# Optimization experiments

Measured on AMD Instinct MI355X. Metric: run time of the kernel, lower is better.

Reference implementation:

```python
import jax, jax.numpy as jnp
import numpy as np

EMBED_DIM = 1024
NUM_HEADS = 16
D_K = EMBED_DIM // NUM_HEADS
MAX_SEQ = 2048
BATCH = 2
SEQ = 2048
ROPE_BASE = 10000.0


def build_rope(seq_len, head_dim, base=ROPE_BASE):
    # standard RoPE: inv_freq over half the head dim, cos/sin of shape [seq, head_dim]
    inv_freq = 1.0 / (base ** (jnp.arange(0, head_dim, 2, dtype=jnp.float32) / head_dim))
    t = jnp.arange(seq_len, dtype=jnp.float32)
    freqs = jnp.einsum('s,d->sd', t, inv_freq)              # [S, D/2]
    emb = jnp.concatenate([freqs, freqs], axis=-1)          # [S, D]
    return jnp.cos(emb), jnp.sin(emb)


def rotate_half(x):
    x1, x2 = jnp.split(x, 2, axis=-1)
    return jnp.concatenate([-x2, x1], axis=-1)


def apply_rope(x, cos, sin):
    # x: [B, H, S, D]; cos/sin: [S, D] -> broadcast over batch & heads
    cos = cos[None, None, :, :]
    sin = sin[None, None, :, :]
    return x * cos + rotate_half(x) * sin


def setup_inputs() -> dict:
    key = jax.random.key(0)
    ks = jax.random.split(key, 9)
    scale = 1.0 / np.sqrt(EMBED_DIM)
    x = jax.random.normal(ks[0], (BATCH, SEQ, EMBED_DIM), dtype=jnp.float32)
    # causal boolean mask, broadcastable to [B, H, S, S]
    mask = jnp.tril(jnp.ones((SEQ, SEQ), dtype=bool))[None, None, :, :]
    cos, sin = build_rope(MAX_SEQ, D_K)
    Wq = jax.random.normal(ks[1], (EMBED_DIM, EMBED_DIM), jnp.float32) * scale
    bq = jnp.zeros((EMBED_DIM,), jnp.float32)
    Wk = jax.random.normal(ks[2], (EMBED_DIM, EMBED_DIM), jnp.float32) * scale
    bk = jnp.zeros((EMBED_DIM,), jnp.float32)
    Wv = jax.random.normal(ks[3], (EMBED_DIM, EMBED_DIM), jnp.float32) * scale
    bv = jnp.zeros((EMBED_DIM,), jnp.float32)
    Wo = jax.random.normal(ks[4], (EMBED_DIM, EMBED_DIM), jnp.float32) * scale
    bo = jnp.zeros((EMBED_DIM,), jnp.float32)
    return {'x': x, 'mask': mask, 'cos': cos, 'sin': sin,
            'Wq': Wq, 'bq': bq, 'Wk': Wk, 'bk': bk, 'Wv': Wv, 'bv': bv,
            'Wo': Wo, 'bo': bo}


def reference(x, mask, cos, sin, Wq, bq, Wk, bk, Wv, bv, Wo, bo):
    B, S, E = x.shape
    H, D = NUM_HEADS, D_K
    # nn.Linear: y = x @ W^T + b
    q = (x @ Wq.T + bq).reshape(B, S, H, D).transpose(0, 2, 1, 3)  # [B,H,S,D]
    k = (x @ Wk.T + bk).reshape(B, S, H, D).transpose(0, 2, 1, 3)
    v = (x @ Wv.T + bv).reshape(B, S, H, D).transpose(0, 2, 1, 3)
    q = apply_rope(q, cos[:S], sin[:S])
    k = apply_rope(k, cos[:S], sin[:S])
    scores = jnp.einsum('bhqd,bhkd->bhqk', q, k) / jnp.sqrt(jnp.float32(D))
    scores = jnp.where(mask, scores, -jnp.inf)
    attn = jax.nn.softmax(scores, axis=-1)
    out = jnp.einsum('bhqk,bhkd->bhqd', attn, v)
    out = out.transpose(0, 2, 1, 3).reshape(B, S, E)
    return out @ Wo.T + bo
```

## Files before the change

### kernel.cpp

```cpp
#include <hip/hip_runtime.h>
#include <hip/hip_bf16.h>
#include <cfloat>
#include <math.h>

#define EMBED 1024
#define NHEADS 16
#define DK 64
#define SEQL 2048
#define BATCH 2
#define NTOK 4096


typedef __bf16 bf16x8 __attribute__((ext_vector_type(8)));
typedef float floatx4 __attribute__((ext_vector_type(4)));

__device__ __forceinline__ unsigned short f2bf(float f) {
    union { __hip_bfloat16 b; unsigned short u; } c;
    c.b = __float2bfloat16(f);
    return c.u;
}

__device__ __forceinline__ void async16(void* lds, const void* g) {
    __builtin_amdgcn_global_load_lds(
        (const __attribute__((address_space(1))) unsigned int*)g,
        (__attribute__((address_space(3))) unsigned int*)lds,
        16, 0, 0);
}

__global__ __launch_bounds__(256) void convert_pack(
    const float* __restrict__ x,  const float* __restrict__ Wq,
    const float* __restrict__ Wk, const float* __restrict__ Wv,
    const float* __restrict__ Wo,
    unsigned short* __restrict__ xb, unsigned short* __restrict__ Wqkv,
    unsigned short* __restrict__ Wob)
{
    const int XG = 1048576, WG = 262144;
    int g = blockIdx.x * 256 + threadIdx.x;
    const float4* s; ushort4* d;
    if (g < XG)               { s = (const float4*)x  + g;                d = (ushort4*)xb   + g; }
    else if (g < XG + WG)     { s = (const float4*)Wq + (g - XG);         d = (ushort4*)Wqkv + (g - XG); }
    else if (g < XG + 2 * WG) { s = (const float4*)Wk + (g - XG - WG);    d = (ushort4*)Wqkv + (g - XG); }
    else if (g < XG + 3 * WG) { s = (const float4*)Wv + (g - XG - 2*WG);  d = (ushort4*)Wqkv + (g - XG); }
    else                      { s = (const float4*)Wo + (g - XG - 3*WG);  d = (ushort4*)Wob  + (g - XG - 3*WG); }
    float4 v = *s;
    *d = (ushort4){f2bf(v.x), f2bf(v.y), f2bf(v.z), f2bf(v.w)};
}

__global__ __launch_bounds__(256) void qkv_gemm(
    const unsigned short* __restrict__ xb, const unsigned short* __restrict__ Wqkv,
    const float* __restrict__ bq, const float* __restrict__ bk, const float* __restrict__ bv,
    const float* __restrict__ cosT, const float* __restrict__ sinT,
    unsigned short* __restrict__ Qg, unsigned short* __restrict__ Kg,
    unsigned short* __restrict__ Vt)
{
    __shared__ __align__(16) unsigned short SM[9216];
    unsigned short* As = SM;
    unsigned short* Bs = SM + 4096;

    const int t = threadIdx.x, lane = t & 63, wave = t >> 6;
    const int quad = lane >> 4, lrow = lane & 15;
    const int m0 = blockIdx.y * 128;
    const int n0 = blockIdx.x * 128;
    const int mw = (wave & 1) * 64, nw = (wave >> 1) * 64;
    const int srow = lane >> 2;
    const int scol = (lane & 3) * 8;

    floatx4 acc[4][4];
    #pragma unroll
    for (int i = 0; i < 4; i++)
        #pragma unroll
        for (int j = 0; j < 4; j++) acc[i][j] = (floatx4){0.f,0.f,0.f,0.f};

    const unsigned short* Ab = xb   + (size_t)(m0 + wave * 32 + srow) * EMBED + scol;
    const unsigned short* Bb = Wqkv + (size_t)(n0 + wave * 32 + srow) * EMBED + scol;

    for (int k0 = 0; k0 < EMBED; k0 += 32) {
        __syncthreads();
        async16(&As[wave * 1024],       Ab + k0);
        async16(&As[wave * 1024 + 512], Ab + 16 * EMBED + k0);
        async16(&Bs[wave * 1024],       Bb + k0);
        async16(&Bs[wave * 1024 + 512], Bb + 16 * EMBED + k0);
        __syncthreads();

        bf16x8 af[4], bfB[4];
        #pragma unroll
        for (int i = 0; i < 4; i++)
            af[i] = *reinterpret_cast<const bf16x8*>(&As[(mw + i * 16 + lrow) * 32 + quad * 8]);
        #pragma unroll
        for (int j = 0; j < 4; j++)
            bfB[j] = *reinterpret_cast<const bf16x8*>(&Bs[(nw + j * 16 + lrow) * 32 + quad * 8]);
        #pragma unroll
        for (int i = 0; i < 4; i++)
            #pragma unroll
            for (int j = 0; j < 4; j++)
                acc[i][j] = __builtin_amdgcn_mfma_f32_16x16x32_bf16(af[i], bfB[j], acc[i][j], 0, 0, 0);
    }

    const int mat  = n0 >> 10;
    const int nloc = n0 & 1023;
    const int bb   = m0 >> 11;
    const int s0   = m0 & (SEQL - 1);

    for (int hn = 0; hn < 2; hn++) {
        const int h = (nloc >> 6) + hn;
        __syncthreads();
        if (mat == 2) {
            unsigned short* T2 = SM;
            if ((wave >> 1) == hn) {
                #pragma unroll
                for (int j = 0; j < 4; j++) {
                    int d = j * 16 + lrow;
                    float bvv = bv[nloc + hn * 64 + d];
                    #pragma unroll
                    for (int i = 0; i < 4; i++) {
                        int tok = mw + i * 16 + quad * 4;
                        *(ushort4*)&T2[d * 136 + tok] = (ushort4){
                            f2bf(acc[i][j][0] + bvv), f2bf(acc[i][j][1] + bvv),
                            f2bf(acc[i][j][2] + bvv), f2bf(acc[i][j][3] + bvv)};
                    }
                }
            }
            __syncthreads();
            int d = t >> 2, tg = (t & 3) * 32;
            unsigned short* dst = Vt + ((size_t)(bb * NHEADS + h) * DK + d) * SEQL + s0 + tg;
            #pragma unroll
            for (int c = 0; c < 32; c += 8)
                *(uint4*)(dst + c) = *(const uint4*)&T2[d * 136 + tg + c];
        } else {
            unsigned short* T = SM;
            const float* bias = (mat == 0) ? bq : bk;
            if ((wave >> 1) == hn) {
                #pragma unroll
                for (int j = 0; j < 4; j++) {
                    int d = j * 16 + lrow;
                    float bvv = bias[nloc + hn * 64 + d];
                    #pragma unroll
                    for (int i = 0; i < 4; i++)
                        #pragma unroll
                        for (int rg = 0; rg < 4; rg++)
                            T[(mw + i * 16 + quad * 4 + rg) * 72 + d] = f2bf(acc[i][j][rg] + bvv);
                }
            }
            __syncthreads();
            int tok = t >> 1, dh = (t & 1) * 32;
            int s = s0 + tok;
            float sgn = dh ? 1.0f : -1.0f;
            unsigned short* dst = ((mat == 0) ? Qg : Kg)
                + ((size_t)(bb * NHEADS + h) * SEQL + s) * DK + dh;
            #pragma unroll
            for (int c = 0; c < 32; c += 8) {
                bf16x8 own = *reinterpret_cast<const bf16x8*>(&T[tok * 72 + dh + c]);
                bf16x8 par = *reinterpret_cast<const bf16x8*>(&T[tok * 72 + (dh ^ 32) + c]);
                float4 c0 = *(const float4*)(cosT + s * DK + dh + c);
                float4 c1 = *(const float4*)(cosT + s * DK + dh + c + 4);
                float4 s0v = *(const float4*)(sinT + s * DK + dh + c);
                float4 s1v = *(const float4*)(sinT + s * DK + dh + c + 4);
                float cv[8] = {c0.x,c0.y,c0.z,c0.w,c1.x,c1.y,c1.z,c1.w};
                float sv[8] = {s0v.x,s0v.y,s0v.z,s0v.w,s1v.x,s1v.y,s1v.z,s1v.w};
                unsigned short o[8];
                #pragma unroll
                for (int e = 0; e < 8; e++)
                    o[e] = f2bf((float)own[e] * cv[e] + sgn * (float)par[e] * sv[e]);
                *(uint4*)(dst + c) = *(const uint4*)o;
            }
        }
    }
}

#define KP 72

__global__ __launch_bounds__(256) void attn_mfma(
    const unsigned short* __restrict__ Qg, const unsigned short* __restrict__ Kg,
    const unsigned short* __restrict__ Vt, unsigned short* __restrict__ CTX)
{
    __shared__ __align__(16) unsigned short Ks[64 * KP];
    __shared__ __align__(16) unsigned short Vs[64 * KP];
    __shared__ __align__(16) unsigned short Ps[64 * KP];

    const int p = blockIdx.x;
    const int h = blockIdx.y, b = blockIdx.z;
    const int qtL = p, qtH = (SEQL / 64 - 1) - p;
    const int t = threadIdx.x;
    const int lane = t & 63, w = t >> 6;
    const int quad = lane >> 4, lrow = lane & 15;
    const int q0L = qtL * 64, q0H = qtH * 64;

    const unsigned short* Qh = Qg + (size_t)(b * NHEADS + h) * SEQL * DK;
    const unsigned short* Kh = Kg + (size_t)(b * NHEADS + h) * SEQL * DK;
    const unsigned short* Vh = Vt + (size_t)(b * NHEADS + h) * DK * SEQL;

    bf16x8 aqL[2], aqH[2];
    #pragma unroll
    for (int ks = 0; ks < 2; ks++) {
        aqL[ks] = *(const bf16x8*)(Qh + (size_t)(q0L + w * 16 + lrow) * DK + quad * 8 + ks * 32);
        aqH[ks] = *(const bf16x8*)(Qh + (size_t)(q0H + w * 16 + lrow) * DK + quad * 8 + ks * 32);
    }

    floatx4 ofL[4], ofH[4];
    float lL[4] = {0,0,0,0}, lH[4] = {0,0,0,0};
    #pragma unroll
    for (int jd = 0; jd < 4; jd++) { ofL[jd] = (floatx4){0,0,0,0}; ofH[jd] = (floatx4){0,0,0,0}; }

    unsigned short* Pw = Ps + w * 16 * KP;

    const int r0 = t >> 3, c8 = (t & 7) * 8;
    uint4 pk0, pk1, pv0, pv1;
    auto pref = [&](int k0) {
        pk0 = *(const uint4*)(Kh + (size_t)(k0 + r0) * DK + c8);
        pk1 = *(const uint4*)(Kh + (size_t)(k0 + r0 + 32) * DK + c8);
        pv0 = *(const uint4*)(Vh + (size_t)r0 * SEQL + k0 + c8);
        pv1 = *(const uint4*)(Vh + (size_t)(r0 + 32) * SEQL + k0 + c8);
    };
    pref(0);

    for (int kt = 0; kt <= qtH; kt++) {
        const int k0 = kt * 64;
        __syncthreads();
        *(uint4*)&Ks[r0 * KP + c8]        = pk0;
        *(uint4*)&Ks[(r0 + 32) * KP + c8] = pk1;
        *(uint4*)&Vs[r0 * KP + c8]        = pv0;
        *(uint4*)&Vs[(r0 + 32) * KP + c8] = pv1;
        __syncthreads();
        if (kt < qtH) pref(k0 + 64);

        {
            floatx4 sc[4];
            #pragma unroll
            for (int j = 0; j < 4; j++) sc[j] = (floatx4){0,0,0,0};
            #pragma unroll
            for (int ks = 0; ks < 2; ks++)
                #pragma unroll
                for (int j = 0; j < 4; j++) {
                    bf16x8 kb = *reinterpret_cast<const bf16x8*>(&Ks[(j * 16 + lrow) * KP + quad * 8 + ks * 32]);
                    sc[j] = __builtin_amdgcn_mfma_f32_16x16x32_bf16(aqH[ks], kb, sc[j], 0, 0, 0);
                }
            const bool diag = (kt == qtH);
            #pragma unroll
            for (int rg = 0; rg < 4; rg++) {
                int row = q0H + w * 16 + quad * 4 + rg;
                float lacc = 0.f;
                #pragma unroll
                for (int j = 0; j < 4; j++) {
                    float pval = __expf(sc[j][rg] * 0.125f);
                    if (diag && (k0 + j * 16 + lrow) > row) pval = 0.f;
                    Pw[(quad * 4 + rg) * KP + j * 16 + lrow] = f2bf(pval);
                    lacc += pval;
                }
                lH[rg] += lacc;
            }
            #pragma unroll
            for (int ks = 0; ks < 2; ks++) {
                bf16x8 pa = *reinterpret_cast<const bf16x8*>(&Pw[lrow * KP + quad * 8 + ks * 32]);
                #pragma unroll
                for (int jd = 0; jd < 4; jd++) {
                    bf16x8 vb = *reinterpret_cast<const bf16x8*>(&Vs[(jd * 16 + lrow) * KP + quad * 8 + ks * 32]);
                    ofH[jd] = __builtin_amdgcn_mfma_f32_16x16x32_bf16(pa, vb, ofH[jd], 0, 0, 0);
                }
            }
        }
        if (kt <= qtL) {
            floatx4 sc[4];
            #pragma unroll
            for (int j = 0; j < 4; j++) sc[j] = (floatx4){0,0,0,0};
            #pragma unroll
            for (int ks = 0; ks < 2; ks++)
                #pragma unroll
                for (int j = 0; j < 4; j++) {
                    bf16x8 kb = *reinterpret_cast<const bf16x8*>(&Ks[(j * 16 + lrow) * KP + quad * 8 + ks * 32]);
                    sc[j] = __builtin_amdgcn_mfma_f32_16x16x32_bf16(aqL[ks], kb, sc[j], 0, 0, 0);
                }
            const bool diag = (kt == qtL);
            #pragma unroll
            for (int rg = 0; rg < 4; rg++) {
                int row = q0L + w * 16 + quad * 4 + rg;
                float lacc = 0.f;
                #pragma unroll
                for (int j = 0; j < 4; j++) {
                    float pval = __expf(sc[j][rg] * 0.125f);
                    if (diag && (k0 + j * 16 + lrow) > row) pval = 0.f;
                    Pw[(quad * 4 + rg) * KP + j * 16 + lrow] = f2bf(pval);
                    lacc += pval;
                }
                lL[rg] += lacc;
            }
            #pragma unroll
            for (int ks = 0; ks < 2; ks++) {
                bf16x8 pa = *reinterpret_cast<const bf16x8*>(&Pw[lrow * KP + quad * 8 + ks * 32]);
                #pragma unroll
                for (int jd = 0; jd < 4; jd++) {
                    bf16x8 vb = *reinterpret_cast<const bf16x8*>(&Vs[(jd * 16 + lrow) * KP + quad * 8 + ks * 32]);
                    ofL[jd] = __builtin_amdgcn_mfma_f32_16x16x32_bf16(pa, vb, ofL[jd], 0, 0, 0);
                }
            }
        }
    }

    #pragma unroll
    for (int rg = 0; rg < 4; rg++) {
        float lv = lH[rg];
        #pragma unroll
        for (int off = 1; off < 16; off <<= 1) lv += __shfl_xor(lv, off);
        float inv = 1.0f / lv;
        int row = q0H + w * 16 + quad * 4 + rg;
        unsigned short* Cr = CTX + ((size_t)(b * NHEADS + h) * SEQL + row) * DK;
        #pragma unroll
        for (int jd = 0; jd < 4; jd++) Cr[jd * 16 + lrow] = f2bf(ofH[jd][rg] * inv);

        lv = lL[rg];
        #pragma unroll
        for (int off = 1; off < 16; off <<= 1) lv += __shfl_xor(lv, off);
        inv = 1.0f / lv;
        row = q0L + w * 16 + quad * 4 + rg;
        Cr = CTX + ((size_t)(b * NHEADS + h) * SEQL + row) * DK;
        #pragma unroll
        for (int jd = 0; jd < 4; jd++) Cr[jd * 16 + lrow] = f2bf(ofL[jd][rg] * inv);
    }
}

__global__ __launch_bounds__(256) void o_gemm(
    const unsigned short* __restrict__ Ag,
    const unsigned short* __restrict__ Bg,
    const float* __restrict__ bias, float* __restrict__ C)
{
    __shared__ __align__(16) unsigned short As[128 * 32];
    __shared__ __align__(16) unsigned short Bs[128 * 32];

    const int t = threadIdx.x, lane = t & 63, wave = t >> 6;
    const int quad = lane >> 4, lrow = lane & 15;
    const int m0 = blockIdx.y * 128, n0 = blockIdx.x * 128;
    const int mw = (wave & 1) * 64, nw = (wave >> 1) * 64;
    const int srow = lane >> 2;
    const int scol = (lane & 3) * 8;

    floatx4 acc[4][4];
    #pragma unroll
    for (int i = 0; i < 4; i++)
        #pragma unroll
        for (int j = 0; j < 4; j++) acc[i][j] = (floatx4){0.f,0.f,0.f,0.f};

    const int tokA0 = m0 + wave * 32 + srow;
    const unsigned short* Bb = Bg + (size_t)(n0 + wave * 32 + srow) * EMBED + scol;

    for (int k0 = 0; k0 < EMBED; k0 += 32) {
        int k = k0 + scol;
        size_t a0 = ((size_t)((tokA0 >> 11) * NHEADS + (k >> 6)) * SEQL + (tokA0 & (SEQL - 1))) * DK + (k & 63);
        int tokA1 = tokA0 + 16;
        size_t a1 = ((size_t)((tokA1 >> 11) * NHEADS + (k >> 6)) * SEQL + (tokA1 & (SEQL - 1))) * DK + (k & 63);
        __syncthreads();
        async16(&As[wave * 1024],       Ag + a0);
        async16(&As[wave * 1024 + 512], Ag + a1);
        async16(&Bs[wave * 1024],       Bb + k0);
        async16(&Bs[wave * 1024 + 512], Bb + 16 * EMBED + k0);
        __syncthreads();

        bf16x8 af[4], bfB[4];
        #pragma unroll
        for (int i = 0; i < 4; i++)
            af[i] = *reinterpret_cast<const bf16x8*>(&As[(mw + i * 16 + lrow) * 32 + quad * 8]);
        #pragma unroll
        for (int j = 0; j < 4; j++)
            bfB[j] = *reinterpret_cast<const bf16x8*>(&Bs[(nw + j * 16 + lrow) * 32 + quad * 8]);
        #pragma unroll
        for (int i = 0; i < 4; i++)
            #pragma unroll
            for (int j = 0; j < 4; j++)
                acc[i][j] = __builtin_amdgcn_mfma_f32_16x16x32_bf16(af[i], bfB[j], acc[i][j], 0, 0, 0);
    }

    #pragma unroll
    for (int i = 0; i < 4; i++)
        #pragma unroll
        for (int rg = 0; rg < 4; rg++) {
            int row_g = m0 + mw + i * 16 + quad * 4 + rg;
            #pragma unroll
            for (int j = 0; j < 4; j++) {
                int col_g = n0 + nw + j * 16 + lrow;
                C[(size_t)row_g * EMBED + col_g] = acc[i][j][rg] + bias[col_g];
            }
        }
}

extern "C" void kernel_launch(void* const* d_in, const int* in_sizes, int n_in,
                              void* d_out, int out_size, void* d_ws, size_t ws_size,
                              hipStream_t stream) {
    const float* x    = (const float*)d_in[0];
    const float* cosT = (const float*)d_in[2];
    const float* sinT = (const float*)d_in[3];
    const float* Wq = (const float*)d_in[4];  const float* bq = (const float*)d_in[5];
    const float* Wk = (const float*)d_in[6];  const float* bk = (const float*)d_in[7];
    const float* Wv = (const float*)d_in[8];  const float* bv = (const float*)d_in[9];
    const float* Wo = (const float*)d_in[10]; const float* bo = (const float*)d_in[11];

    const size_t MB = 1024 * 1024;
    char* ws = (char*)d_ws;
    unsigned short* xb   = (unsigned short*)(ws);
    unsigned short* Wqkv = (unsigned short*)(ws +  8 * MB);
    unsigned short* Wob  = (unsigned short*)(ws + 14 * MB);
    unsigned short* Qg   = (unsigned short*)(ws + 16 * MB);
    unsigned short* Kg   = (unsigned short*)(ws + 24 * MB);
    unsigned short* Vt   = (unsigned short*)(ws + 32 * MB);
    unsigned short* CTXb = (unsigned short*)(ws + 40 * MB);

    convert_pack<<<8192, 256, 0, stream>>>(x, Wq, Wk, Wv, Wo, xb, Wqkv, Wob);

    dim3 qkv_grid(3 * EMBED / 128, NTOK / 128);
    qkv_gemm<<<qkv_grid, 256, 0, stream>>>(xb, Wqkv, bq, bk, bv, cosT, sinT, Qg, Kg, Vt);

    dim3 attn_grid(SEQL / 128, NHEADS, BATCH);
    attn_mfma<<<attn_grid, 256, 0, stream>>>(Qg, Kg, Vt, CTXb);

    dim3 o_grid(EMBED / 128, NTOK / 128);
    o_gemm<<<o_grid, 256, 0, stream>>>(CTXb, Wob, bo, (float*)d_out);
}
```

Measured before the change: 255.7 us.

## Double K-step in GEMMs and widen attention KV tile to 128 keys

The QKV and output-projection GEMMs now stage 64 elements of K per barrier pair (two 32-wide LDS sub-tiles) instead of 32, halving the number of synchronisation rounds. The attention kernel now processes 128 keys per iteration, with eight score fragments per wave and wider padded V and P tiles, halving the loop trip count and barriers. In exchange, LDS use per block grows, which may reduce occupancy. Register pressure also rises from more prefetch registers and score accumulators. The diagonal tile can also do up to 64 keys of fully masked, wasted work.

```diff
diff --git a/kernel.cpp b/kernel.cpp
--- a/kernel.cpp
+++ b/kernel.cpp
@@ -53,9 +53,11 @@
     unsigned short* __restrict__ Qg, unsigned short* __restrict__ Kg,
     unsigned short* __restrict__ Vt)
 {
-    __shared__ __align__(16) unsigned short SM[9216];
-    unsigned short* As = SM;
-    unsigned short* Bs = SM + 4096;
+    __shared__ __align__(16) unsigned short SM[16384];
+    unsigned short* As0 = SM;
+    unsigned short* As1 = SM + 4096;
+    unsigned short* Bs0 = SM + 8192;
+    unsigned short* Bs1 = SM + 12288;
 
     const int t = threadIdx.x, lane = t & 63, wave = t >> 6;
     const int quad = lane >> 4, lrow = lane & 15;
@@ -71,29 +73,36 @@
         #pragma unroll
         for (int j = 0; j < 4; j++) acc[i][j] = (floatx4){0.f,0.f,0.f,0.f};
 
-    const unsigned short* Ab = xb   + (size_t)(m0 + wave * 32 + srow) * EMBED + scol;
-    const unsigned short* Bb = Wqkv + (size_t)(n0 + wave * 32 + srow) * EMBED + scol;
-
-    for (int k0 = 0; k0 < EMBED; k0 += 32) {
-        __syncthreads();
-        async16(&As[wave * 1024],       Ab + k0);
-        async16(&As[wave * 1024 + 512], Ab + 16 * EMBED + k0);
-        async16(&Bs[wave * 1024],       Bb + k0);
-        async16(&Bs[wave * 1024 + 512], Bb + 16 * EMBED + k0);
-        __syncthreads();
-
-        bf16x8 af[4], bfB[4];
-        #pragma unroll
-        for (int i = 0; i < 4; i++)
-            af[i] = *reinterpret_cast<const bf16x8*>(&As[(mw + i * 16 + lrow) * 32 + quad * 8]);
-        #pragma unroll
-        for (int j = 0; j < 4; j++)
-            bfB[j] = *reinterpret_cast<const bf16x8*>(&Bs[(nw + j * 16 + lrow) * 32 + quad * 8]);
-        #pragma unroll
-        for (int i = 0; i < 4; i++)
+    for (int k0 = 0; k0 < EMBED; k0 += 64) {
+        __syncthreads();
+        #pragma unroll
+        for (int c = 0; c < 2; c++) {
+            const unsigned short* as = xb   + (size_t)(m0 + wave * 32 + c * 16 + srow) * EMBED + k0 + scol;
+            const unsigned short* bs = Wqkv + (size_t)(n0 + wave * 32 + c * 16 + srow) * EMBED + k0 + scol;
+            async16(&As0[wave * 1024 + c * 512], as);
+            async16(&As1[wave * 1024 + c * 512], as + 32);
+            async16(&Bs0[wave * 1024 + c * 512], bs);
+            async16(&Bs1[wave * 1024 + c * 512], bs + 32);
+        }
+        __syncthreads();
+
+        #pragma unroll
+        for (int ks = 0; ks < 2; ks++) {
+            const unsigned short* Ab = ks ? As1 : As0;
+            const unsigned short* Bb = ks ? Bs1 : Bs0;
+            bf16x8 af[4], bfB[4];
+            #pragma unroll
+            for (int i = 0; i < 4; i++)
+                af[i] = *reinterpret_cast<const bf16x8*>(&Ab[(mw + i * 16 + lrow) * 32 + quad * 8]);
             #pragma unroll
             for (int j = 0; j < 4; j++)
-                acc[i][j] = __builtin_amdgcn_mfma_f32_16x16x32_bf16(af[i], bfB[j], acc[i][j], 0, 0, 0);
+                bfB[j] = *reinterpret_cast<const bf16x8*>(&Bb[(nw + j * 16 + lrow) * 32 + quad * 8]);
+            #pragma unroll
+            for (int i = 0; i < 4; i++)
+                #pragma unroll
+                for (int j = 0; j < 4; j++)
+                    acc[i][j] = __builtin_amdgcn_mfma_f32_16x16x32_bf16(af[i], bfB[j], acc[i][j], 0, 0, 0);
+        }
     }
 
     const int mat  = n0 >> 10;
@@ -168,14 +177,15 @@
 }
 
 #define KP 72
+#define VP 136
 
 __global__ __launch_bounds__(256) void attn_mfma(
     const unsigned short* __restrict__ Qg, const unsigned short* __restrict__ Kg,
     const unsigned short* __restrict__ Vt, unsigned short* __restrict__ CTX)
 {
-    __shared__ __align__(16) unsigned short Ks[64 * KP];
-    __shared__ __align__(16) unsigned short Vs[64 * KP];
-    __shared__ __align__(16) unsigned short Ps[64 * KP];
+    __shared__ __align__(16) unsigned short Ks[128 * KP];
+    __shared__ __align__(16) unsigned short Vs[64 * VP];
+    __shared__ __align__(16) unsigned short Ps[64 * VP];
 
     const int p = blockIdx.x;
     const int h = blockIdx.y, b = blockIdx.z;
@@ -184,6 +194,7 @@
     const int lane = t & 63, w = t >> 6;
     const int quad = lane >> 4, lrow = lane & 15;
     const int q0L = qtL * 64, q0H = qtH * 64;
+    const int ktHmax = qtH >> 1, ktLmax = qtL >> 1;
 
     const unsigned short* Qh = Qg + (size_t)(b * NHEADS + h) * SEQL * DK;
     const unsigned short* Kh = Kg + (size_t)(b * NHEADS + h) * SEQL * DK;
@@ -201,94 +212,97 @@
     #pragma unroll
     for (int jd = 0; jd < 4; jd++) { ofL[jd] = (floatx4){0,0,0,0}; ofH[jd] = (floatx4){0,0,0,0}; }
 
-    unsigned short* Pw = Ps + w * 16 * KP;
-
-    const int r0 = t >> 3, c8 = (t & 7) * 8;
-    uint4 pk0, pk1, pv0, pv1;
+    unsigned short* Pw = Ps + w * 16 * VP;
+
+    const int kr = t >> 3, kc8 = (t & 7) * 8;
+    const int vr = t >> 4, vc8 = (t & 15) * 8;
+    uint4 pk[4], pv[4];
     auto pref = [&](int k0) {
-        pk0 = *(const uint4*)(Kh + (size_t)(k0 + r0) * DK + c8);
-        pk1 = *(const uint4*)(Kh + (size_t)(k0 + r0 + 32) * DK + c8);
-        pv0 = *(const uint4*)(Vh + (size_t)r0 * SEQL + k0 + c8);
-        pv1 = *(const uint4*)(Vh + (size_t)(r0 + 32) * SEQL + k0 + c8);
+        #pragma unroll
+        for (int n = 0; n < 4; n++) {
+            pk[n] = *(const uint4*)(Kh + (size_t)(k0 + kr + 32 * n) * DK + kc8);
+            pv[n] = *(const uint4*)(Vh + (size_t)(vr + 16 * n) * SEQL + k0 + vc8);
+        }
     };
     pref(0);
 
-    for (int kt = 0; kt <= qtH; kt++) {
-        const int k0 = kt * 64;
-        __syncthreads();
-        *(uint4*)&Ks[r0 * KP + c8]        = pk0;
-        *(uint4*)&Ks[(r0 + 32) * KP + c8] = pk1;
-        *(uint4*)&Vs[r0 * KP + c8]        = pv0;
-        *(uint4*)&Vs[(r0 + 32) * KP + c8] = pv1;
-        __syncthreads();
-        if (kt < qtH) pref(k0 + 64);
+    for (int kt = 0; kt <= ktHmax; kt++) {
+        const int k0 = kt * 128;
+        __syncthreads();
+        #pragma unroll
+        for (int n = 0; n < 4; n++) {
+            *(uint4*)&Ks[(kr + 32 * n) * KP + kc8] = pk[n];
+            *(uint4*)&Vs[(vr + 16 * n) * VP + vc8] = pv[n];
+        }
+        __syncthreads();
+        if (kt < ktHmax) pref(k0 + 128);
 
         {
-            floatx4 sc[4];
-            #pragma unroll
-            for (int j = 0; j < 4; j++) sc[j] = (floatx4){0,0,0,0};
+            floatx4 sc[8];
+            #pragma unroll
+            for (int j = 0; j < 8; j++) sc[j] = (floatx4){0,0,0,0};
             #pragma unroll
             for (int ks = 0; ks < 2; ks++)
                 #pragma unroll
-                for (int j = 0; j < 4; j++) {
+                for (int j = 0; j < 8; j++) {
                     bf16x8 kb = *reinterpret_cast<const bf16x8*>(&Ks[(j * 16 + lrow) * KP + quad * 8 + ks * 32]);
                     sc[j] = __builtin_amdgcn_mfma_f32_16x16x32_bf16(aqH[ks], kb, sc[j], 0, 0, 0);
                 }
-            const bool diag = (kt == qtH);
+            const bool diag = (kt == ktHmax);
             #pragma unroll
             for (int rg = 0; rg < 4; rg++) {
                 int row = q0H + w * 16 + quad * 4 + rg;
                 float lacc = 0.f;
                 #pragma unroll
-                for (int j = 0; j < 4; j++) {
+                for (int j = 0; j < 8; j++) {
                     float pval = __expf(sc[j][rg] * 0.125f);
                     if (diag && (k0 + j * 16 + lrow) > row) pval = 0.f;
-                    Pw[(quad * 4 + rg) * KP + j * 16 + lrow] = f2bf(pval);
+                    Pw[(quad * 4 + rg) * VP + j * 16 + lrow] = f2bf(pval);
                     lacc += pval;
                 }
                 lH[rg] += lacc;
             }
             #pragma unroll
-            for (int ks = 0; ks < 2; ks++) {
-                bf16x8 pa = *reinterpret_cast<const bf16x8*>(&Pw[lrow * KP + quad * 8 + ks * 32]);
+            for (int ks = 0; ks < 4; ks++) {
+                bf16x8 pa = *reinterpret_cast<const bf16x8*>(&Pw[lrow * VP + quad * 8 + ks * 32]);
                 #pragma unroll
                 for (int jd = 0; jd < 4; jd++) {
-                    bf16x8 vb = *reinterpret_cast<const bf16x8*>(&Vs[(jd * 16 + lrow) * KP + quad * 8 + ks * 32]);
+                    bf16x8 vb = *reinterpret_cast<const bf16x8*>(&Vs[(jd * 16 + lrow) * VP + quad * 8 + ks * 32]);
                     ofH[jd] = __builtin_amdgcn_mfma_f32_16x16x32_bf16(pa, vb, ofH[jd], 0, 0, 0);
                 }
             }
         }
-        if (kt <= qtL) {
-            floatx4 sc[4];
-            #pragma unroll
-            for (int j = 0; j < 4; j++) sc[j] = (floatx4){0,0,0,0};
+        if (kt <= ktLmax) {
+            floatx4 sc[8];
+            #pragma unroll
+            for (int j = 0; j < 8; j++) sc[j] = (floatx4){0,0,0,0};
             #pragma unroll
             for (int ks = 0; ks < 2; ks++)
                 #pragma unroll
-                for (int j = 0; j < 4; j++) {
+                for (int j = 0; j < 8; j++) {
                     bf16x8 kb = *reinterpret_cast<const bf16x8*>(&Ks[(j * 16 + lrow) * KP + quad * 8 + ks * 32]);
                     sc[j] = __builtin_amdgcn_mfma_f32_16x16x32_bf16(aqL[ks], kb, sc[j], 0, 0, 0);
                 }
-            const bool diag = (kt == qtL);
+            const bool diag = (kt == ktLmax);
             #pragma unroll
             for (int rg = 0; rg < 4; rg++) {
                 int row = q0L + w * 16 + quad * 4 + rg;
                 float lacc = 0.f;
                 #pragma unroll
-                for (int j = 0; j < 4; j++) {
+                for (int j = 0; j < 8; j++) {
                     float pval = __expf(sc[j][rg] * 0.125f);
                     if (diag && (k0 + j * 16 + lrow) > row) pval = 0.f;
-                    Pw[(quad * 4 + rg) * KP + j * 16 + lrow] = f2bf(pval);
+                    Pw[(quad * 4 + rg) * VP + j * 16 + lrow] = f2bf(pval);
                     lacc += pval;
                 }
                 lL[rg] += lacc;
             }
             #pragma unroll
-            for (int ks = 0; ks < 2; ks++) {
-                bf16x8 pa = *reinterpret_cast<const bf16x8*>(&Pw[lrow * KP + quad * 8 + ks * 32]);
+            for (int ks = 0; ks < 4; ks++) {
+                bf16x8 pa = *reinterpret_cast<const bf16x8*>(&Pw[lrow * VP + quad * 8 + ks * 32]);
                 #pragma unroll
                 for (int jd = 0; jd < 4; jd++) {
-                    bf16x8 vb = *reinterpret_cast<const bf16x8*>(&Vs[(jd * 16 + lrow) * KP + quad * 8 + ks * 32]);
+                    bf16x8 vb = *reinterpret_cast<const bf16x8*>(&Vs[(jd * 16 + lrow) * VP + quad * 8 + ks * 32]);
                     ofL[jd] = __builtin_amdgcn_mfma_f32_16x16x32_bf16(pa, vb, ofL[jd], 0, 0, 0);
                 }
             }
@@ -322,8 +336,11 @@
     const unsigned short* __restrict__ Bg,
     const float* __restrict__ bias, float* __restrict__ C)
 {
-    __shared__ __align__(16) unsigned short As[128 * 32];
-    __shared__ __align__(16) unsigned short Bs[128 * 32];
+    __shared__ __align__(16) unsigned short SM[16384];
+    unsigned short* As0 = SM;
+    unsigned short* As1 = SM + 4096;
+    unsigned short* Bs0 = SM + 8192;
+    unsigned short* Bs1 = SM + 12288;
 
     const int t = threadIdx.x, lane = t & 63, wave = t >> 6;
     const int quad = lane >> 4, lrow = lane & 15;
@@ -338,33 +355,39 @@
         #pragma unroll
         for (int j = 0; j < 4; j++) acc[i][j] = (floatx4){0.f,0.f,0.f,0.f};
 
-    const int tokA0 = m0 + wave * 32 + srow;
-    const unsigned short* Bb = Bg + (size_t)(n0 + wave * 32 + srow) * EMBED + scol;
-
-    for (int k0 = 0; k0 < EMBED; k0 += 32) {
-        int k = k0 + scol;
-        size_t a0 = ((size_t)((tokA0 >> 11) * NHEADS + (k >> 6)) * SEQL + (tokA0 & (SEQL - 1))) * DK + (k & 63);
-        int tokA1 = tokA0 + 16;
-        size_t a1 = ((size_t)((tokA1 >> 11) * NHEADS + (k >> 6)) * SEQL + (tokA1 & (SEQL - 1))) * DK + (k & 63);
-        __syncthreads();
-        async16(&As[wave * 1024],       Ag + a0);
-        async16(&As[wave * 1024 + 512], Ag + a1);
-        async16(&Bs[wave * 1024],       Bb + k0);
-        async16(&Bs[wave * 1024 + 512], Bb + 16 * EMBED + k0);
-        __syncthreads();
-
-        bf16x8 af[4], bfB[4];
-        #pragma unroll
-        for (int i = 0; i < 4; i++)
-            af[i] = *reinterpret_cast<const bf16x8*>(&As[(mw + i * 16 + lrow) * 32 + quad * 8]);
-        #pragma unroll
-        for (int j = 0; j < 4; j++)
-            bfB[j] = *reinterpret_cast<const bf16x8*>(&Bs[(nw + j * 16 + lrow) * 32 + quad * 8]);
-        #pragma unroll
-        for (int i = 0; i < 4; i++)
+    for (int k0 = 0; k0 < EMBED; k0 += 64) {
+        const int hh = k0 >> 6;
+        __syncthreads();
+        #pragma unroll
+        for (int c = 0; c < 2; c++) {
+            int tok = m0 + wave * 32 + c * 16 + srow;
+            const unsigned short* as = Ag
+                + ((size_t)((tok >> 11) * NHEADS + hh) * SEQL + (tok & (SEQL - 1))) * DK + scol;
+            const unsigned short* bs = Bg + (size_t)(n0 + wave * 32 + c * 16 + srow) * EMBED + k0 + scol;
+            async16(&As0[wave * 1024 + c * 512], as);
+            async16(&As1[wave * 1024 + c * 512], as + 32);
+            async16(&Bs0[wave * 1024 + c * 512], bs);
+            async16(&Bs1[wave * 1024 + c * 512], bs + 32);
+        }
+        __syncthreads();
+
+        #pragma unroll
+        for (int ks = 0; ks < 2; ks++) {
+            const unsigned short* Ab = ks ? As1 : As0;
+            const unsigned short* Bb = ks ? Bs1 : Bs0;
+            bf16x8 af[4], bfB[4];
+            #pragma unroll
+            for (int i = 0; i < 4; i++)
+                af[i] = *reinterpret_cast<const bf16x8*>(&Ab[(mw + i * 16 + lrow) * 32 + quad * 8]);
             #pragma unroll
             for (int j = 0; j < 4; j++)
-                acc[i][j] = __builtin_amdgcn_mfma_f32_16x16x32_bf16(af[i], bfB[j], acc[i][j], 0, 0, 0);
+                bfB[j] = *reinterpret_cast<const bf16x8*>(&Bb[(nw + j * 16 + lrow) * 32 + quad * 8]);
+            #pragma unroll
+            for (int i = 0; i < 4; i++)
+                #pragma unroll
+                for (int j = 0; j < 4; j++)
+                    acc[i][j] = __builtin_amdgcn_mfma_f32_16x16x32_bf16(af[i], bfB[j], acc[i][j], 0, 0, 0);
+        }
     }
 
     #pragma unroll
```

After: 290.4 us. 13.6% more time.

## Shrink GEMM tiles to 128x64 with K=64 steps and unpair attention query tiles

Applied to the files above, without the earlier changes.

Both GEMMs move from 128x128 tiles with K-step 32 to 128x64 tiles with K-step 64. This doubles the block count and halves the number of barrier pairs per K. The attention kernel no longer pairs a low and a high query tile per block; each block handles one 64-row tile, longest first. The grid doubles, raising occupancy and parallelism on the large CU count, at the cost of less data reuse per block and a load imbalance that the reversed launch order is meant to offset.

```diff
diff --git a/kernel.cpp b/kernel.cpp
--- a/kernel.cpp
+++ b/kernel.cpp
@@ -53,116 +53,118 @@
     unsigned short* __restrict__ Qg, unsigned short* __restrict__ Kg,
     unsigned short* __restrict__ Vt)
 {
-    __shared__ __align__(16) unsigned short SM[9216];
-    unsigned short* As = SM;
-    unsigned short* Bs = SM + 4096;
+    __shared__ __align__(16) unsigned short SM[12288];
+    unsigned short* As0 = SM;
+    unsigned short* As1 = SM + 4096;
+    unsigned short* Bs0 = SM + 8192;
+    unsigned short* Bs1 = SM + 10240;
 
     const int t = threadIdx.x, lane = t & 63, wave = t >> 6;
     const int quad = lane >> 4, lrow = lane & 15;
     const int m0 = blockIdx.y * 128;
-    const int n0 = blockIdx.x * 128;
-    const int mw = (wave & 1) * 64, nw = (wave >> 1) * 64;
+    const int n0 = blockIdx.x * 64;
     const int srow = lane >> 2;
     const int scol = (lane & 3) * 8;
 
-    floatx4 acc[4][4];
-    #pragma unroll
-    for (int i = 0; i < 4; i++)
+    floatx4 acc[2][4];
+    #pragma unroll
+    for (int i = 0; i < 2; i++)
         #pragma unroll
         for (int j = 0; j < 4; j++) acc[i][j] = (floatx4){0.f,0.f,0.f,0.f};
 
-    const unsigned short* Ab = xb   + (size_t)(m0 + wave * 32 + srow) * EMBED + scol;
-    const unsigned short* Bb = Wqkv + (size_t)(n0 + wave * 32 + srow) * EMBED + scol;
-
-    for (int k0 = 0; k0 < EMBED; k0 += 32) {
-        __syncthreads();
-        async16(&As[wave * 1024],       Ab + k0);
-        async16(&As[wave * 1024 + 512], Ab + 16 * EMBED + k0);
-        async16(&Bs[wave * 1024],       Bb + k0);
-        async16(&Bs[wave * 1024 + 512], Bb + 16 * EMBED + k0);
-        __syncthreads();
-
-        bf16x8 af[4], bfB[4];
-        #pragma unroll
-        for (int i = 0; i < 4; i++)
-            af[i] = *reinterpret_cast<const bf16x8*>(&As[(mw + i * 16 + lrow) * 32 + quad * 8]);
-        #pragma unroll
-        for (int j = 0; j < 4; j++)
-            bfB[j] = *reinterpret_cast<const bf16x8*>(&Bs[(nw + j * 16 + lrow) * 32 + quad * 8]);
-        #pragma unroll
-        for (int i = 0; i < 4; i++)
+    for (int k0 = 0; k0 < EMBED; k0 += 64) {
+        __syncthreads();
+        #pragma unroll
+        for (int c = 0; c < 2; c++) {
+            const unsigned short* as = xb + (size_t)(m0 + wave * 32 + c * 16 + srow) * EMBED + k0 + scol;
+            async16(&As0[wave * 1024 + c * 512], as);
+            async16(&As1[wave * 1024 + c * 512], as + 32);
+        }
+        const unsigned short* bs = Wqkv + (size_t)(n0 + wave * 16 + srow) * EMBED + k0 + scol;
+        async16(&Bs0[wave * 512], bs);
+        async16(&Bs1[wave * 512], bs + 32);
+        __syncthreads();
+
+        #pragma unroll
+        for (int ks = 0; ks < 2; ks++) {
+            const unsigned short* Ab = ks ? As1 : As0;
+            const unsigned short* Bb = ks ? Bs1 : Bs0;
+            bf16x8 af[2], bfB[4];
+            #pragma unroll
+            for (int i = 0; i < 2; i++)
+                af[i] = *reinterpret_cast<const bf16x8*>(&Ab[(wave * 32 + i * 16 + lrow) * 32 + quad * 8]);
             #pragma unroll
             for (int j = 0; j < 4; j++)
-                acc[i][j] = __builtin_amdgcn_mfma_f32_16x16x32_bf16(af[i], bfB[j], acc[i][j], 0, 0, 0);
+                bfB[j] = *reinterpret_cast<const bf16x8*>(&Bb[(j * 16 + lrow) * 32 + quad * 8]);
+            #pragma unroll
+            for (int i = 0; i < 2; i++)
+                #pragma unroll
+                for (int j = 0; j < 4; j++)
+                    acc[i][j] = __builtin_amdgcn_mfma_f32_16x16x32_bf16(af[i], bfB[j], acc[i][j], 0, 0, 0);
+        }
     }
 
     const int mat  = n0 >> 10;
     const int nloc = n0 & 1023;
+    const int h    = nloc >> 6;
     const int bb   = m0 >> 11;
     const int s0   = m0 & (SEQL - 1);
 
-    for (int hn = 0; hn < 2; hn++) {
-        const int h = (nloc >> 6) + hn;
-        __syncthreads();
-        if (mat == 2) {
-            unsigned short* T2 = SM;
-            if ((wave >> 1) == hn) {
+    __syncthreads();
+    if (mat == 2) {
+        unsigned short* T2 = SM;
+        #pragma unroll
+        for (int j = 0; j < 4; j++) {
+            int d = j * 16 + lrow;
+            float bvv = bv[nloc + d];
+            #pragma unroll
+            for (int i = 0; i < 2; i++) {
+                int tok = wave * 32 + i * 16 + quad * 4;
+                *(ushort4*)&T2[d * 136 + tok] = (ushort4){
+                    f2bf(acc[i][j][0] + bvv), f2bf(acc[i][j][1] + bvv),
+                    f2bf(acc[i][j][2] + bvv), f2bf(acc[i][j][3] + bvv)};
+            }
+        }
+        __syncthreads();
+        int d = t >> 2, tg = (t & 3) * 32;
+        unsigned short* dst = Vt + ((size_t)(bb * NHEADS + h) * DK + d) * SEQL + s0 + tg;
+        #pragma unroll
+        for (int c = 0; c < 32; c += 8)
+            *(uint4*)(dst + c) = *(const uint4*)&T2[d * 136 + tg + c];
+    } else {
+        unsigned short* T = SM;
+        const float* bias = (mat == 0) ? bq : bk;
+        #pragma unroll
+        for (int j = 0; j < 4; j++) {
+            int d = j * 16 + lrow;
+            float bvv = bias[nloc + d];
+            #pragma unroll
+            for (int i = 0; i < 2; i++)
                 #pragma unroll
-                for (int j = 0; j < 4; j++) {
-                    int d = j * 16 + lrow;
-                    float bvv = bv[nloc + hn * 64 + d];
-                    #pragma unroll
-                    for (int i = 0; i < 4; i++) {
-                        int tok = mw + i * 16 + quad * 4;
-                        *(ushort4*)&T2[d * 136 + tok] = (ushort4){
-                            f2bf(acc[i][j][0] + bvv), f2bf(acc[i][j][1] + bvv),
-                            f2bf(acc[i][j][2] + bvv), f2bf(acc[i][j][3] + bvv)};
-                    }
-                }
-            }
-            __syncthreads();
-            int d = t >> 2, tg = (t & 3) * 32;
-            unsigned short* dst = Vt + ((size_t)(bb * NHEADS + h) * DK + d) * SEQL + s0 + tg;
-            #pragma unroll
-            for (int c = 0; c < 32; c += 8)
-                *(uint4*)(dst + c) = *(const uint4*)&T2[d * 136 + tg + c];
-        } else {
-            unsigned short* T = SM;
-            const float* bias = (mat == 0) ? bq : bk;
-            if ((wave >> 1) == hn) {
-                #pragma unroll
-                for (int j = 0; j < 4; j++) {
-                    int d = j * 16 + lrow;
-                    float bvv = bias[nloc + hn * 64 + d];
-                    #pragma unroll
-                    for (int i = 0; i < 4; i++)
-                        #pragma unroll
-                        for (int rg = 0; rg < 4; rg++)
-                            T[(mw + i * 16 + quad * 4 + rg) * 72 + d] = f2bf(acc[i][j][rg] + bvv);
-                }
-            }
-            __syncthreads();
-            int tok = t >> 1, dh = (t & 1) * 32;
-            int s = s0 + tok;
-            float sgn = dh ? 1.0f : -1.0f;
-            unsigned short* dst = ((mat == 0) ? Qg : Kg)
-                + ((size_t)(bb * NHEADS + h) * SEQL + s) * DK + dh;
-            #pragma unroll
-            for (int c = 0; c < 32; c += 8) {
-                bf16x8 own = *reinterpret_cast<const bf16x8*>(&T[tok * 72 + dh + c]);
-                bf16x8 par = *reinterpret_cast<const bf16x8*>(&T[tok * 72 + (dh ^ 32) + c]);
-                float4 c0 = *(const float4*)(cosT + s * DK + dh + c);
-                float4 c1 = *(const float4*)(cosT + s * DK + dh + c + 4);
-                float4 s0v = *(const float4*)(sinT + s * DK + dh + c);
-                float4 s1v = *(const float4*)(sinT + s * DK + dh + c + 4);
-                float cv[8] = {c0.x,c0.y,c0.z,c0.w,c1.x,c1.y,c1.z,c1.w};
-                float sv[8] = {s0v.x,s0v.y,s0v.z,s0v.w,s1v.x,s1v.y,s1v.z,s1v.w};
-                unsigned short o[8];
-                #pragma unroll
-                for (int e = 0; e < 8; e++)
-                    o[e] = f2bf((float)own[e] * cv[e] + sgn * (float)par[e] * sv[e]);
-                *(uint4*)(dst + c) = *(const uint4*)o;
-            }
+                for (int rg = 0; rg < 4; rg++)
+                    T[(wave * 32 + i * 16 + quad * 4 + rg) * 72 + d] = f2bf(acc[i][j][rg] + bvv);
+        }
+        __syncthreads();
+        int tok = t >> 1, dh = (t & 1) * 32;
+        int s = s0 + tok;
+        float sgn = dh ? 1.0f : -1.0f;
+        unsigned short* dst = ((mat == 0) ? Qg : Kg)
+            + ((size_t)(bb * NHEADS + h) * SEQL + s) * DK + dh;
+        #pragma unroll
+        for (int c = 0; c < 32; c += 8) {
+            bf16x8 own = *reinterpret_cast<const bf16x8*>(&T[tok * 72 + dh + c]);
+            bf16x8 par = *reinterpret_cast<const bf16x8*>(&T[tok * 72 + (dh ^ 32) + c]);
+            float4 c0 = *(const float4*)(cosT + s * DK + dh + c);
+            float4 c1 = *(const float4*)(cosT + s * DK + dh + c + 4);
+            float4 s0v = *(const float4*)(sinT + s * DK + dh + c);
+            float4 s1v = *(const float4*)(sinT + s * DK + dh + c + 4);
+            float cv[8] = {c0.x,c0.y,c0.z,c0.w,c1.x,c1.y,c1.z,c1.w};
+            float sv[8] = {s0v.x,s0v.y,s0v.z,s0v.w,s1v.x,s1v.y,s1v.z,s1v.w};
+            unsigned short o[8];
+            #pragma unroll
+            for (int e = 0; e < 8; e++)
+                o[e] = f2bf((float)own[e] * cv[e] + sgn * (float)par[e] * sv[e]);
+            *(uint4*)(dst + c) = *(const uint4*)o;
         }
     }
 }
@@ -177,29 +179,26 @@
     __shared__ __align__(16) unsigned short Vs[64 * KP];
     __shared__ __align__(16) unsigned short Ps[64 * KP];
 
-    const int p = blockIdx.x;
+    const int qt = (SEQL / 64 - 1) - blockIdx.x;
     const int h = blockIdx.y, b = blockIdx.z;
-    const int qtL = p, qtH = (SEQL / 64 - 1) - p;
     const int t = threadIdx.x;
     const int lane = t & 63, w = t >> 6;
     const int quad = lane >> 4, lrow = lane & 15;
-    const int q0L = qtL * 64, q0H = qtH * 64;
+    const int q0 = qt * 64;
 
     const unsigned short* Qh = Qg + (size_t)(b * NHEADS + h) * SEQL * DK;
     const unsigned short* Kh = Kg + (size_t)(b * NHEADS + h) * SEQL * DK;
     const unsigned short* Vh = Vt + (size_t)(b * NHEADS + h) * DK * SEQL;
 
-    bf16x8 aqL[2], aqH[2];
-    #pragma unroll
-    for (int ks = 0; ks < 2; ks++) {
-        aqL[ks] = *(const bf16x8*)(Qh + (size_t)(q0L + w * 16 + lrow) * DK + quad * 8 + ks * 32);
-        aqH[ks] = *(const bf16x8*)(Qh + (size_t)(q0H + w * 16 + lrow) * DK + quad * 8 + ks * 32);
-    }
-
-    floatx4 ofL[4], ofH[4];
-    float lL[4] = {0,0,0,0}, lH[4] = {0,0,0,0};
-    #pragma unroll
-    for (int jd = 0; jd < 4; jd++) { ofL[jd] = (floatx4){0,0,0,0}; ofH[jd] = (floatx4){0,0,0,0}; }
+    bf16x8 aq[2];
+    #pragma unroll
+    for (int ks = 0; ks < 2; ks++)
+        aq[ks] = *(const bf16x8*)(Qh + (size_t)(q0 + w * 16 + lrow) * DK + quad * 8 + ks * 32);
+
+    floatx4 of[4];
+    float l[4] = {0,0,0,0};
+    #pragma unroll
+    for (int jd = 0; jd < 4; jd++) of[jd] = (floatx4){0,0,0,0};
 
     unsigned short* Pw = Ps + w * 16 * KP;
 
@@ -213,7 +212,7 @@
     };
     pref(0);
 
-    for (int kt = 0; kt <= qtH; kt++) {
+    for (int kt = 0; kt <= qt; kt++) {
         const int k0 = kt * 64;
         __syncthreads();
         *(uint4*)&Ks[r0 * KP + c8]        = pk0;
@@ -221,99 +220,54 @@
         *(uint4*)&Vs[r0 * KP + c8]        = pv0;
         *(uint4*)&Vs[(r0 + 32) * KP + c8] = pv1;
         __syncthreads();
-        if (kt < qtH) pref(k0 + 64);
-
-        {
-            floatx4 sc[4];
-            #pragma unroll
-            for (int j = 0; j < 4; j++) sc[j] = (floatx4){0,0,0,0};
-            #pragma unroll
-            for (int ks = 0; ks < 2; ks++)
-                #pragma unroll
-                for (int j = 0; j < 4; j++) {
-                    bf16x8 kb = *reinterpret_cast<const bf16x8*>(&Ks[(j * 16 + lrow) * KP + quad * 8 + ks * 32]);
-                    sc[j] = __builtin_amdgcn_mfma_f32_16x16x32_bf16(aqH[ks], kb, sc[j], 0, 0, 0);
-                }
-            const bool diag = (kt == qtH);
-            #pragma unroll
-            for (int rg = 0; rg < 4; rg++) {
-                int row = q0H + w * 16 + quad * 4 + rg;
-                float lacc = 0.f;
-                #pragma unroll
-                for (int j = 0; j < 4; j++) {
-                    float pval = __expf(sc[j][rg] * 0.125f);
-                    if (diag && (k0 + j * 16 + lrow) > row) pval = 0.f;
-                    Pw[(quad * 4 + rg) * KP + j * 16 + lrow] = f2bf(pval);
-                    lacc += pval;
-                }
-                lH[rg] += lacc;
-            }
-            #pragma unroll
-            for (int ks = 0; ks < 2; ks++) {
-                bf16x8 pa = *reinterpret_cast<const bf16x8*>(&Pw[lrow * KP + quad * 8 + ks * 32]);
-                #pragma unroll
-                for (int jd = 0; jd < 4; jd++) {
-                    bf16x8 vb = *reinterpret_cast<const bf16x8*>(&Vs[(jd * 16 + lrow) * KP + quad * 8 + ks * 32]);
-                    ofH[jd] = __builtin_amdgcn_mfma_f32_16x16x32_bf16(pa, vb, ofH[jd], 0, 0, 0);
-                }
-            }
-        }
-        if (kt <= qtL) {
-            floatx4 sc[4];
-            #pragma unroll
-            for (int j = 0; j < 4; j++) sc[j] = (floatx4){0,0,0,0};
-            #pragma unroll
-            for (int ks = 0; ks < 2; ks++)
-                #pragma unroll
-                for (int j = 0; j < 4; j++) {
-                    bf16x8 kb = *reinterpret_cast<const bf16x8*>(&Ks[(j * 16 + lrow) * KP + quad * 8 + ks * 32]);
-                    sc[j] = __builtin_amdgcn_mfma_f32_16x16x32_bf16(aqL[ks], kb, sc[j], 0, 0, 0);
-                }
-            const bool diag = (kt == qtL);
-            #pragma unroll
-            for (int rg = 0; rg < 4; rg++) {
-                int row = q0L + w * 16 + quad * 4 + rg;
-                float lacc = 0.f;
-                #pragma unroll
-                for (int j = 0; j < 4; j++) {
-                    float pval = __expf(sc[j][rg] * 0.125f);
-                    if (diag && (k0 + j * 16 + lrow) > row) pval = 0.f;
-                    Pw[(quad * 4 + rg) * KP + j * 16 + lrow] = f2bf(pval);
-                    lacc += pval;
-                }
-                lL[rg] += lacc;
-            }
-            #pragma unroll
-            for (int ks = 0; ks < 2; ks++) {
-                bf16x8 pa = *reinterpret_cast<const bf16x8*>(&Pw[lrow * KP + quad * 8 + ks * 32]);
-                #pragma unroll
-                for (int jd = 0; jd < 4; jd++) {
-                    bf16x8 vb = *reinterpret_cast<const bf16x8*>(&Vs[(jd * 16 + lrow) * KP + quad * 8 + ks * 32]);
-                    ofL[jd] = __builtin_amdgcn_mfma_f32_16x16x32_bf16(pa, vb, ofL[jd], 0, 0, 0);
-                }
+        if (kt < qt) pref(k0 + 64);
+
+        floatx4 sc[4];
+        #pragma unroll
+        for (int j = 0; j < 4; j++) sc[j] = (floatx4){0,0,0,0};
+        #pragma unroll
+        for (int ks = 0; ks < 2; ks++)
+            #pragma unroll
+            for (int j = 0; j < 4; j++) {
+                bf16x8 kb = *reinterpret_cast<const bf16x8*>(&Ks[(j * 16 + lrow) * KP + quad * 8 + ks * 32]);
+                sc[j] = __builtin_amdgcn_mfma_f32_16x16x32_bf16(aq[ks], kb, sc[j], 0, 0, 0);
+            }
+
+        const bool diag = (kt == qt);
+        #pragma unroll
+        for (int rg = 0; rg < 4; rg++) {
+            int row = q0 + w * 16 + quad * 4 + rg;
+            float lacc = 0.f;
+            #pragma unroll
+            for (int j = 0; j < 4; j++) {
+                float pval = __expf(sc[j][rg] * 0.125f);
+                if (diag && (k0 + j * 16 + lrow) > row) pval = 0.f;
+                Pw[(quad * 4 + rg) * KP + j * 16 + lrow] = f2bf(pval);
+                lacc += pval;
+            }
+            l[rg] += lacc;
+        }
+        #pragma unroll
+        for (int ks = 0; ks < 2; ks++) {
+            bf16x8 pa = *reinterpret_cast<const bf16x8*>(&Pw[lrow * KP + quad * 8 + ks * 32]);
+            #pragma unroll
+            for (int jd = 0; jd < 4; jd++) {
+                bf16x8 vb = *reinterpret_cast<const bf16x8*>(&Vs[(jd * 16 + lrow) * KP + quad * 8 + ks * 32]);
+                of[jd] = __builtin_amdgcn_mfma_f32_16x16x32_bf16(pa, vb, of[jd], 0, 0, 0);
             }
         }
     }
 
     #pragma unroll
     for (int rg = 0; rg < 4; rg++) {
-        float lv = lH[rg];
+        float lv = l[rg];
         #pragma unroll
         for (int off = 1; off < 16; off <<= 1) lv += __shfl_xor(lv, off);
         float inv = 1.0f / lv;
-        int row = q0H + w * 16 + quad * 4 + rg;
+        int row = q0 + w * 16 + quad * 4 + rg;
         unsigned short* Cr = CTX + ((size_t)(b * NHEADS + h) * SEQL + row) * DK;
         #pragma unroll
-        for (int jd = 0; jd < 4; jd++) Cr[jd * 16 + lrow] = f2bf(ofH[jd][rg] * inv);
-
-        lv = lL[rg];
-        #pragma unroll
-        for (int off = 1; off < 16; off <<= 1) lv += __shfl_xor(lv, off);
-        inv = 1.0f / lv;
-        row = q0L + w * 16 + quad * 4 + rg;
-        Cr = CTX + ((size_t)(b * NHEADS + h) * SEQL + row) * DK;
-        #pragma unroll
-        for (int jd = 0; jd < 4; jd++) Cr[jd * 16 + lrow] = f2bf(ofL[jd][rg] * inv);
+        for (int jd = 0; jd < 4; jd++) Cr[jd * 16 + lrow] = f2bf(of[jd][rg] * inv);
     }
 }
 
@@ -322,59 +276,67 @@
     const unsigned short* __restrict__ Bg,
     const float* __restrict__ bias, float* __restrict__ C)
 {
-    __shared__ __align__(16) unsigned short As[128 * 32];
-    __shared__ __align__(16) unsigned short Bs[128 * 32];
+    __shared__ __align__(16) unsigned short SM[12288];
+    unsigned short* As0 = SM;
+    unsigned short* As1 = SM + 4096;
+    unsigned short* Bs0 = SM + 8192;
+    unsigned short* Bs1 = SM + 10240;
 
     const int t = threadIdx.x, lane = t & 63, wave = t >> 6;
     const int quad = lane >> 4, lrow = lane & 15;
-    const int m0 = blockIdx.y * 128, n0 = blockIdx.x * 128;
-    const int mw = (wave & 1) * 64, nw = (wave >> 1) * 64;
+    const int m0 = blockIdx.y * 128, n0 = blockIdx.x * 64;
     const int srow = lane >> 2;
     const int scol = (lane & 3) * 8;
 
-    floatx4 acc[4][4];
-    #pragma unroll
-    for (int i = 0; i < 4; i++)
+    floatx4 acc[2][4];
+    #pragma unroll
+    for (int i = 0; i < 2; i++)
         #pragma unroll
         for (int j = 0; j < 4; j++) acc[i][j] = (floatx4){0.f,0.f,0.f,0.f};
 
-    const int tokA0 = m0 + wave * 32 + srow;
-    const unsigned short* Bb = Bg + (size_t)(n0 + wave * 32 + srow) * EMBED + scol;
-
-    for (int k0 = 0; k0 < EMBED; k0 += 32) {
-        int k = k0 + scol;
-        size_t a0 = ((size_t)((tokA0 >> 11) * NHEADS + (k >> 6)) * SEQL + (tokA0 & (SEQL - 1))) * DK + (k & 63);
-        int tokA1 = tokA0 + 16;
-        size_t a1 = ((size_t)((tokA1 >> 11) * NHEADS + (k >> 6)) * SEQL + (tokA1 & (SEQL - 1))) * DK + (k & 63);
-        __syncthreads();
-        async16(&As[wave * 1024],       Ag + a0);
-        async16(&As[wave * 1024 + 512], Ag + a1);
-        async16(&Bs[wave * 1024],       Bb + k0);
-        async16(&Bs[wave * 1024 + 512], Bb + 16 * EMBED + k0);
-        __syncthreads();
-
-        bf16x8 af[4], bfB[4];
-        #pragma unroll
-        for (int i = 0; i < 4; i++)
-            af[i] = *reinterpret_cast<const bf16x8*>(&As[(mw + i * 16 + lrow) * 32 + quad * 8]);
-        #pragma unroll
-        for (int j = 0; j < 4; j++)
-            bfB[j] = *reinterpret_cast<const bf16x8*>(&Bs[(nw + j * 16 + lrow) * 32 + quad * 8]);
-        #pragma unroll
-        for (int i = 0; i < 4; i++)
+    for (int k0 = 0; k0 < EMBED; k0 += 64) {
+        const int hh = k0 >> 6;
+        __syncthreads();
+        #pragma unroll
+        for (int c = 0; c < 2; c++) {
+            int tok = m0 + wave * 32 + c * 16 + srow;
+            const unsigned short* as = Ag
+                + ((size_t)((tok >> 11) * NHEADS + hh) * SEQL + (tok & (SEQL - 1))) * DK + scol;
+            async16(&As0[wave * 1024 + c * 512], as);
+            async16(&As1[wave * 1024 + c * 512], as + 32);
+        }
+        const unsigned short* bs = Bg + (size_t)(n0 + wave * 16 + srow) * EMBED + k0 + scol;
+        async16(&Bs0[wave * 512], bs);
+        async16(&Bs1[wave * 512], bs + 32);
+        __syncthreads();
+
+        #pragma unroll
+        for (int ks = 0; ks < 2; ks++) {
+            const unsigned short* Ab = ks ? As1 : As0;
+            const unsigned short* Bb = ks ? Bs1 : Bs0;
+            bf16x8 af[2], bfB[4];
+            #pragma unroll
+            for (int i = 0; i < 2; i++)
+                af[i] = *reinterpret_cast<const bf16x8*>(&Ab[(wave * 32 + i * 16 + lrow) * 32 + quad * 8]);
             #pragma unroll
             for (int j = 0; j < 4; j++)
-                acc[i][j] = __builtin_amdgcn_mfma_f32_16x16x32_bf16(af[i], bfB[j], acc[i][j], 0, 0, 0);
-    }
-
-    #pragma unroll
-    for (int i = 0; i < 4; i++)
+                bfB[j] = *reinterpret_cast<const bf16x8*>(&Bb[(j * 16 + lrow) * 32 + quad * 8]);
+            #pragma unroll
+            for (int i = 0; i < 2; i++)
+                #pragma unroll
+                for (int j = 0; j < 4; j++)
+                    acc[i][j] = __builtin_amdgcn_mfma_f32_16x16x32_bf16(af[i], bfB[j], acc[i][j], 0, 0, 0);
+        }
+    }
+
+    #pragma unroll
+    for (int i = 0; i < 2; i++)
         #pragma unroll
         for (int rg = 0; rg < 4; rg++) {
-            int row_g = m0 + mw + i * 16 + quad * 4 + rg;
+            int row_g = m0 + wave * 32 + i * 16 + quad * 4 + rg;
             #pragma unroll
             for (int j = 0; j < 4; j++) {
-                int col_g = n0 + nw + j * 16 + lrow;
+                int col_g = n0 + j * 16 + lrow;
                 C[(size_t)row_g * EMBED + col_g] = acc[i][j][rg] + bias[col_g];
             }
         }
@@ -403,12 +365,12 @@
 
     convert_pack<<<8192, 256, 0, stream>>>(x, Wq, Wk, Wv, Wo, xb, Wqkv, Wob);
 
-    dim3 qkv_grid(3 * EMBED / 128, NTOK / 128);
+    dim3 qkv_grid(3 * EMBED / 64, NTOK / 128);
     qkv_gemm<<<qkv_grid, 256, 0, stream>>>(xb, Wqkv, bq, bk, bv, cosT, sinT, Qg, Kg, Vt);
 
-    dim3 attn_grid(SEQL / 128, NHEADS, BATCH);
+    dim3 attn_grid(SEQL / 64, NHEADS, BATCH);
     attn_mfma<<<attn_grid, 256, 0, stream>>>(Qg, Kg, Vt, CTXb);
 
-    dim3 o_grid(EMBED / 128, NTOK / 128);
+    dim3 o_grid(EMBED / 64, NTOK / 128);
     o_gemm<<<o_grid, 256, 0, stream>>>(CTXb, Wob, bo, (float*)d_out);
 }
```

Result: faster. 235.9 us, median of 2 (-7.7%).
